# Kernel optimization log

Hardware: AMD Instinct MI355X
Metric: run time of the kernel (lower is better)

## Reference

```python
import jax, jax.numpy as jnp
import numpy as np

B, SQ, SK, H, A = 4, 512, 512, 256, 128

def setup_inputs() -> dict:
    key = jax.random.key(0)
    ks = jax.random.split(key, 8)
    s = 1.0 / np.sqrt(H)
    sa = 1.0 / np.sqrt(A)
    return {
        "Q": jax.random.normal(ks[0], (B, SQ, H), dtype=jnp.float32),
        "K": jax.random.normal(ks[1], (B, SK, H), dtype=jnp.float32),
        "V": jax.random.normal(ks[2], (B, SK, H), dtype=jnp.float32),
        "W_q": jax.random.uniform(ks[3], (H, A), jnp.float32, -s, s),
        "W_k": jax.random.uniform(ks[4], (H, A), jnp.float32, -s, s),
        "v": jax.random.uniform(ks[5], (A,), jnp.float32, -sa, sa),
        "W_o": jax.random.uniform(ks[6], (H, H), jnp.float32, -s, s),
        "b_o": jax.random.uniform(ks[7], (H,), jnp.float32, -s, s),
    }

def reference(Q, K, V, W_q, W_k, v, W_o, b_o):
    # Q: (B, Sq, H), K/V: (B, Sk, H)
    Qt = Q @ W_q                      # (B, Sq, A)
    Kt = K @ W_k                      # (B, Sk, A)
    additive = jnp.tanh(Qt[:, :, None, :] + Kt[:, None, :, :])  # (B, Sq, Sk, A)
    scores = jnp.einsum('bqka,a->bqk', additive, v)             # (B, Sq, Sk)
    weights = jax.nn.softmax(scores, axis=-1)                   # (B, Sq, Sk)
    out = jnp.einsum('bqk,bkh->bqh', weights, V)                 # (B, Sq, H)
    out = out @ W_o + b_o
    return (out, weights)
```

## Files before the change

kernel.cpp:

```cpp
#include <hip/hip_runtime.h>
#include <math.h>

#define BB 4
#define SQL 512
#define SKL 512
#define HH 256
#define AA 128

#define PRESCALE 2.8853900817779268f

__device__ inline void fma4(float4& a, float s, const float4& b) {
    a.x = fmaf(s, b.x, a.x); a.y = fmaf(s, b.y, a.y);
    a.z = fmaf(s, b.z, a.z); a.w = fmaf(s, b.w, a.w);
}

__global__ __launch_bounds__(256) void prep_kernel(
    const float* __restrict__ Q, const float* __restrict__ K,
    const float* __restrict__ V,
    const float* __restrict__ Wq, const float* __restrict__ Wk,
    const float* __restrict__ Wo,
    float* __restrict__ Qt, float* __restrict__ Kt, float* __restrict__ VW)
{
    __shared__ float rows[16 * HH];
    __shared__ float wl[64 * 128];
    int tid = threadIdx.x;
    int bid = blockIdx.x;

    const float* X; const float* W; float* Y;
    int ldW, ldY, col0, r0; float scale;
    if (bid < 128)      { X=Q; W=Wq; Y=Qt; ldW=AA; ldY=AA; col0=0; r0=bid*16;       scale=PRESCALE; }
    else if (bid < 256) { X=K; W=Wk; Y=Kt; ldW=AA; ldY=AA; col0=0; r0=(bid-128)*16; scale=PRESCALE; }
    else { int b2=bid-256; X=V; W=Wo; Y=VW; ldW=HH; ldY=HH; col0=(b2&1)*128; r0=(b2>>1)*16; scale=1.0f; }

    {
        const float4* Xv = (const float4*)(X + (size_t)r0 * HH);
        float4* rv = (float4*)rows;
        rv[tid]       = Xv[tid];
        rv[tid + 256] = Xv[tid + 256];
        rv[tid + 512] = Xv[tid + 512];
        rv[tid + 768] = Xv[tid + 768];
    }

    int r  = tid >> 5;
    int c4 = tid & 31;
    float4 accA = {0.f,0.f,0.f,0.f}, accB = {0.f,0.f,0.f,0.f};

    for (int ch = 0; ch < 4; ++ch) {
        __syncthreads();
        {
            const float* Wbase = W + (size_t)(ch * 64) * ldW + col0;
            float4* wv = (float4*)wl;
            #pragma unroll
            for (int it = 0; it < 8; ++it) {
                int l = tid + it * 256;
                wv[l] = *(const float4*)(Wbase + (size_t)(l >> 5) * ldW + ((l & 31) << 2));
            }
        }
        __syncthreads();
        const float* rrowA = rows + r * HH + ch * 64;
        const float* rrowB = rows + (r + 8) * HH + ch * 64;
        #pragma unroll 4
        for (int h4 = 0; h4 < 16; ++h4) {
            float4 ra = *(const float4*)(rrowA + h4 * 4);
            float4 rb = *(const float4*)(rrowB + h4 * 4);
            const float* wbase = wl + (h4 * 4) * 128 + (c4 << 2);
            float4 w0 = *(const float4*)(wbase);
            float4 w1 = *(const float4*)(wbase + 128);
            float4 w2 = *(const float4*)(wbase + 256);
            float4 w3 = *(const float4*)(wbase + 384);
            fma4(accA, ra.x, w0); fma4(accA, ra.y, w1);
            fma4(accA, ra.z, w2); fma4(accA, ra.w, w3);
            fma4(accB, rb.x, w0); fma4(accB, rb.y, w1);
            fma4(accB, rb.z, w2); fma4(accB, rb.w, w3);
        }
    }
    accA.x *= scale; accA.y *= scale; accA.z *= scale; accA.w *= scale;
    accB.x *= scale; accB.y *= scale; accB.z *= scale; accB.w *= scale;
    *(float4*)(Y + (size_t)(r0 + r)     * ldY + col0 + (c4 << 2)) = accA;
    *(float4*)(Y + (size_t)(r0 + r + 8) * ldY + col0 + (c4 << 2)) = accB;
}

__global__ __launch_bounds__(256) void score_kernel(
    const float* __restrict__ Qt, const float* __restrict__ Kt,
    const float* __restrict__ v,  const float* __restrict__ VW,
    const float* __restrict__ bo,
    float* __restrict__ weights,  float* __restrict__ out)
{
    __shared__ float score[2][SKL];
    __shared__ float pout[4][2][HH];

    int tid = threadIdx.x;
    int b  = blockIdx.x >> 8;
    int q0 = (blockIdx.x & 255) << 1;
    int ag = tid & 7;
    int kl = tid >> 3;

    float qreg0[16], qreg1[16], v2reg[16];
    {
        const float4* vp  = (const float4*)(v + ag * 16);
        const float4* qp0 = (const float4*)(Qt + (size_t)(b * SQL + q0)     * AA + ag * 16);
        const float4* qp1 = (const float4*)(Qt + (size_t)(b * SQL + q0 + 1) * AA + ag * 16);
        #pragma unroll
        for (int j4 = 0; j4 < 4; ++j4) {
            float4 vv4 = vp[j4];
            *(float4*)&qreg0[j4 * 4] = qp0[j4];
            *(float4*)&qreg1[j4 * 4] = qp1[j4];
            v2reg[j4 * 4 + 0] = 2.0f * vv4.x;
            v2reg[j4 * 4 + 1] = 2.0f * vv4.y;
            v2reg[j4 * 4 + 2] = 2.0f * vv4.z;
            v2reg[j4 * 4 + 3] = 2.0f * vv4.w;
        }
    }

    float S_all;
    {
        float ls = 0.f;
        #pragma unroll
        for (int j = 0; j < 16; ++j) ls += v2reg[j];
        ls += __shfl_xor(ls, 1);
        ls += __shfl_xor(ls, 2);
        ls += __shfl_xor(ls, 4);
        S_all = 0.5f * ls;
    }

    for (int c = 0; c < 16; ++c) {
        int k = c * 32 + kl;
        const float4* kt4 = (const float4*)(Kt + (size_t)(b * SKL + k) * AA + ag * 16);
        float kt[16];
        *(float4*)&kt[0]  = kt4[0];
        *(float4*)&kt[4]  = kt4[1];
        *(float4*)&kt[8]  = kt4[2];
        *(float4*)&kt[12] = kt4[3];

        float p0 = 0.f, p1 = 0.f;
        #pragma unroll
        for (int j = 0; j < 16; ++j) {
            float kv = kt[j];
            float x0 = qreg0[j] + kv;
            float x1 = qreg1[j] + kv;
            float e0 = __builtin_amdgcn_exp2f(x0);
            float e1 = __builtin_amdgcn_exp2f(x1);
            float r0 = __builtin_amdgcn_rcpf(e0 + 1.0f);
            float r1 = __builtin_amdgcn_rcpf(e1 + 1.0f);
            p0 = fmaf(v2reg[j], r0, p0);
            p1 = fmaf(v2reg[j], r1, p1);
        }
        p0 += __shfl_xor(p0, 1); p1 += __shfl_xor(p1, 1);
        p0 += __shfl_xor(p0, 2); p1 += __shfl_xor(p1, 2);
        p0 += __shfl_xor(p0, 4); p1 += __shfl_xor(p1, 4);
        if (ag == 0) {
            score[0][k] = S_all - p0;
            score[1][k] = S_all - p1;
        }
    }
    __syncthreads();

    int wave = tid >> 6, lane = tid & 63;
    if (wave < 2) {
        int qi = wave;
        float m = -1e30f;
        for (int k = lane; k < SKL; k += 64) m = fmaxf(m, score[qi][k]);
        #pragma unroll
        for (int off = 32; off; off >>= 1) m = fmaxf(m, __shfl_xor(m, off));
        float s = 0.f;
        for (int k = lane; k < SKL; k += 64) {
            float e = __builtin_amdgcn_exp2f((score[qi][k] - m) * 1.44269504f);
            score[qi][k] = e;
            s += e;
        }
        #pragma unroll
        for (int off = 32; off; off >>= 1) s += __shfl_xor(s, off);
        float rinv = 1.0f / s;
        size_t rowoff = (size_t)(b * SQL + q0 + qi) * SKL;
        for (int k = lane; k < SKL; k += 64) {
            float wv2 = score[qi][k] * rinv;
            score[qi][k] = wv2;
            weights[rowoff + k] = wv2;
        }
    }
    __syncthreads();

    {
        const float4* VWb = (const float4*)(VW + (size_t)b * SKL * HH);
        float4 a0 = {0,0,0,0}, a1 = {0,0,0,0};
        int kbase = wave * 128;
        #pragma unroll 4
        for (int k = 0; k < 128; ++k) {
            int kk = kbase + k;
            float4 vw4 = VWb[kk * (HH / 4) + lane];
            float w0 = score[0][kk];
            float w1 = score[1][kk];
            fma4(a0, w0, vw4);
            fma4(a1, w1, vw4);
        }
        *(float4*)&pout[wave][0][lane << 2] = a0;
        *(float4*)&pout[wave][1][lane << 2] = a1;
    }
    __syncthreads();
    {
        int h = tid;
        float bias = bo[h];
        #pragma unroll
        for (int qi = 0; qi < 2; ++qi) {
            float s = bias + pout[0][qi][h] + pout[1][qi][h]
                           + pout[2][qi][h] + pout[3][qi][h];
            out[(size_t)(b * SQL + q0 + qi) * HH + h] = s;
        }
    }
}

extern "C" void kernel_launch(void* const* d_in, const int* in_sizes, int n_in,
                              void* d_out, int out_size, void* d_ws, size_t ws_size,
                              hipStream_t stream)
{
    const float* Q  = (const float*)d_in[0];
    const float* K  = (const float*)d_in[1];
    const float* V  = (const float*)d_in[2];
    const float* Wq = (const float*)d_in[3];
    const float* Wk = (const float*)d_in[4];
    const float* v  = (const float*)d_in[5];
    const float* Wo = (const float*)d_in[6];
    const float* bo = (const float*)d_in[7];

    float* out     = (float*)d_out;
    float* weights = out + (size_t)BB * SQL * HH;

    float* Qt = (float*)d_ws;
    float* Kt = Qt + (size_t)BB * SQL * AA;
    float* VW = Kt + (size_t)BB * SKL * AA;

    prep_kernel <<<512, 256, 0, stream>>>(Q, K, V, Wq, Wk, Wo, Qt, Kt, VW);
    score_kernel<<<1024, 256, 0, stream>>>(Qt, Kt, v, VW, bo, weights, out);
}
```

Measured before the change: 129.8 us.

## Share exp across query pair, store VW in bf16, prefetch loads, parallelize softmax

In the score loop the second query's exp is computed as the first query's exp times a precomputed exp(q1-q0) factor, which removes one transcendental per element. Kt rows and W chunks are register-prefetched one iteration ahead to overlap loads with compute. The V@Wo intermediate is stored as bf16 to halve its memory traffic, at some cost in precision. Softmax now uses all four waves with float4 accesses and shared-memory partial reductions. The factored exp can overflow or lose accuracy when the two query rows differ a lot.

```diff
diff --git a/kernel.cpp b/kernel.cpp
--- a/kernel.cpp
+++ b/kernel.cpp
@@ -14,23 +14,37 @@
     a.z = fmaf(s, b.z, a.z); a.w = fmaf(s, b.w, a.w);
 }
 
+__device__ inline unsigned short f_to_bf16(float f) {
+    unsigned u = __float_as_uint(f);
+    return (unsigned short)((u + 0x7fffu + ((u >> 16) & 1u)) >> 16);
+}
+__device__ inline float4 bf16x4_to_f4(uint2 u) {
+    float4 r;
+    r.x = __uint_as_float(u.x << 16);
+    r.y = __uint_as_float(u.x & 0xffff0000u);
+    r.z = __uint_as_float(u.y << 16);
+    r.w = __uint_as_float(u.y & 0xffff0000u);
+    return r;
+}
+
 __global__ __launch_bounds__(256) void prep_kernel(
     const float* __restrict__ Q, const float* __restrict__ K,
     const float* __restrict__ V,
     const float* __restrict__ Wq, const float* __restrict__ Wk,
     const float* __restrict__ Wo,
-    float* __restrict__ Qt, float* __restrict__ Kt, float* __restrict__ VW)
+    float* __restrict__ Qt, float* __restrict__ Kt,
+    unsigned short* __restrict__ VW)
 {
     __shared__ float rows[16 * HH];
     __shared__ float wl[64 * 128];
     int tid = threadIdx.x;
     int bid = blockIdx.x;
 
-    const float* X; const float* W; float* Y;
-    int ldW, ldY, col0, r0; float scale;
-    if (bid < 128)      { X=Q; W=Wq; Y=Qt; ldW=AA; ldY=AA; col0=0; r0=bid*16;       scale=PRESCALE; }
-    else if (bid < 256) { X=K; W=Wk; Y=Kt; ldW=AA; ldY=AA; col0=0; r0=(bid-128)*16; scale=PRESCALE; }
-    else { int b2=bid-256; X=V; W=Wo; Y=VW; ldW=HH; ldY=HH; col0=(b2&1)*128; r0=(b2>>1)*16; scale=1.0f; }
+    const float* X; const float* W;
+    int ldW, col0, r0; float scale;
+    if (bid < 128)      { X=Q; W=Wq; ldW=AA; col0=0; r0=bid*16;       scale=PRESCALE; }
+    else if (bid < 256) { X=K; W=Wk; ldW=AA; col0=0; r0=(bid-128)*16; scale=PRESCALE; }
+    else { int b2=bid-256; X=V; W=Wo; ldW=HH; col0=(b2&1)*128; r0=(b2>>1)*16; scale=1.0f; }
 
     {
         const float4* Xv = (const float4*)(X + (size_t)r0 * HH);
@@ -41,6 +55,16 @@
         rv[tid + 768] = Xv[tid + 768];
     }
 
+    float4 wpf[8];
+    {
+        const float* Wb = W + col0;
+        #pragma unroll
+        for (int it = 0; it < 8; ++it) {
+            int l = tid + it * 256;
+            wpf[it] = *(const float4*)(Wb + (size_t)(l >> 5) * ldW + ((l & 31) << 2));
+        }
+    }
+
     int r  = tid >> 5;
     int c4 = tid & 31;
     float4 accA = {0.f,0.f,0.f,0.f}, accB = {0.f,0.f,0.f,0.f};
@@ -48,12 +72,16 @@
     for (int ch = 0; ch < 4; ++ch) {
         __syncthreads();
         {
-            const float* Wbase = W + (size_t)(ch * 64) * ldW + col0;
             float4* wv = (float4*)wl;
             #pragma unroll
-            for (int it = 0; it < 8; ++it) {
-                int l = tid + it * 256;
-                wv[l] = *(const float4*)(Wbase + (size_t)(l >> 5) * ldW + ((l & 31) << 2));
+            for (int it = 0; it < 8; ++it) wv[tid + it * 256] = wpf[it];
+            if (ch < 3) {
+                const float* Wb = W + (size_t)((ch + 1) * 64) * ldW + col0;
+                #pragma unroll
+                for (int it = 0; it < 8; ++it) {
+                    int l = tid + it * 256;
+                    wpf[it] = *(const float4*)(Wb + (size_t)(l >> 5) * ldW + ((l & 31) << 2));
+                }
             }
         }
         __syncthreads();
@@ -74,20 +102,32 @@
             fma4(accB, rb.z, w2); fma4(accB, rb.w, w3);
         }
     }
-    accA.x *= scale; accA.y *= scale; accA.z *= scale; accA.w *= scale;
-    accB.x *= scale; accB.y *= scale; accB.z *= scale; accB.w *= scale;
-    *(float4*)(Y + (size_t)(r0 + r)     * ldY + col0 + (c4 << 2)) = accA;
-    *(float4*)(Y + (size_t)(r0 + r + 8) * ldY + col0 + (c4 << 2)) = accB;
+
+    if (bid < 256) {
+        float* Y = (bid < 128) ? Qt : Kt;
+        accA.x *= scale; accA.y *= scale; accA.z *= scale; accA.w *= scale;
+        accB.x *= scale; accB.y *= scale; accB.z *= scale; accB.w *= scale;
+        *(float4*)(Y + (size_t)(r0 + r)     * AA + (c4 << 2)) = accA;
+        *(float4*)(Y + (size_t)(r0 + r + 8) * AA + (c4 << 2)) = accB;
+    } else {
+        ushort4 sa = { f_to_bf16(accA.x), f_to_bf16(accA.y),
+                       f_to_bf16(accA.z), f_to_bf16(accA.w) };
+        ushort4 sb = { f_to_bf16(accB.x), f_to_bf16(accB.y),
+                       f_to_bf16(accB.z), f_to_bf16(accB.w) };
+        *(ushort4*)(VW + (size_t)(r0 + r)     * HH + col0 + (c4 << 2)) = sa;
+        *(ushort4*)(VW + (size_t)(r0 + r + 8) * HH + col0 + (c4 << 2)) = sb;
+    }
 }
 
 __global__ __launch_bounds__(256) void score_kernel(
     const float* __restrict__ Qt, const float* __restrict__ Kt,
-    const float* __restrict__ v,  const float* __restrict__ VW,
+    const float* __restrict__ v,  const unsigned short* __restrict__ VW,
     const float* __restrict__ bo,
     float* __restrict__ weights,  float* __restrict__ out)
 {
     __shared__ float score[2][SKL];
     __shared__ float pout[4][2][HH];
+    __shared__ float pm[2][2], ps[2][2];
 
     int tid = threadIdx.x;
     int b  = blockIdx.x >> 8;
@@ -95,7 +135,7 @@
     int ag = tid & 7;
     int kl = tid >> 3;
 
-    float qreg0[16], qreg1[16], v2reg[16];
+    float qreg0[16], dreg[16], v2reg[16];
     {
         const float4* vp  = (const float4*)(v + ag * 16);
         const float4* qp0 = (const float4*)(Qt + (size_t)(b * SQL + q0)     * AA + ag * 16);
@@ -103,12 +143,17 @@
         #pragma unroll
         for (int j4 = 0; j4 < 4; ++j4) {
             float4 vv4 = vp[j4];
-            *(float4*)&qreg0[j4 * 4] = qp0[j4];
-            *(float4*)&qreg1[j4 * 4] = qp1[j4];
-            v2reg[j4 * 4 + 0] = 2.0f * vv4.x;
-            v2reg[j4 * 4 + 1] = 2.0f * vv4.y;
-            v2reg[j4 * 4 + 2] = 2.0f * vv4.z;
-            v2reg[j4 * 4 + 3] = 2.0f * vv4.w;
+            float4 a0  = qp0[j4];
+            float4 a1  = qp1[j4];
+            *(float4*)&qreg0[j4 * 4] = a0;
+            dreg[j4*4+0] = __builtin_amdgcn_exp2f(a1.x - a0.x);
+            dreg[j4*4+1] = __builtin_amdgcn_exp2f(a1.y - a0.y);
+            dreg[j4*4+2] = __builtin_amdgcn_exp2f(a1.z - a0.z);
+            dreg[j4*4+3] = __builtin_amdgcn_exp2f(a1.w - a0.w);
+            v2reg[j4*4+0] = 2.0f * vv4.x;
+            v2reg[j4*4+1] = 2.0f * vv4.y;
+            v2reg[j4*4+2] = 2.0f * vv4.z;
+            v2reg[j4*4+3] = 2.0f * vv4.w;
         }
     }
 
@@ -123,23 +168,25 @@
         S_all = 0.5f * ls;
     }
 
+    const float4* kp = (const float4*)(Kt + (size_t)(b * SKL + kl) * AA + ag * 16);
+    float4 n0 = kp[0], n1 = kp[1], n2 = kp[2], n3 = kp[3];
     for (int c = 0; c < 16; ++c) {
-        int k = c * 32 + kl;
-        const float4* kt4 = (const float4*)(Kt + (size_t)(b * SKL + k) * AA + ag * 16);
         float kt[16];
-        *(float4*)&kt[0]  = kt4[0];
-        *(float4*)&kt[4]  = kt4[1];
-        *(float4*)&kt[8]  = kt4[2];
-        *(float4*)&kt[12] = kt4[3];
+        *(float4*)&kt[0]  = n0;
+        *(float4*)&kt[4]  = n1;
+        *(float4*)&kt[8]  = n2;
+        *(float4*)&kt[12] = n3;
+        if (c < 15) {
+            const float4* np = kp + (size_t)(c + 1) * 32 * (AA / 4);
+            n0 = np[0]; n1 = np[1]; n2 = np[2]; n3 = np[3];
+        }
 
         float p0 = 0.f, p1 = 0.f;
         #pragma unroll
         for (int j = 0; j < 16; ++j) {
-            float kv = kt[j];
-            float x0 = qreg0[j] + kv;
-            float x1 = qreg1[j] + kv;
+            float x0 = qreg0[j] + kt[j];
             float e0 = __builtin_amdgcn_exp2f(x0);
-            float e1 = __builtin_amdgcn_exp2f(x1);
+            float e1 = e0 * dreg[j];
             float r0 = __builtin_amdgcn_rcpf(e0 + 1.0f);
             float r1 = __builtin_amdgcn_rcpf(e1 + 1.0f);
             p0 = fmaf(v2reg[j], r0, p0);
@@ -149,6 +196,7 @@
         p0 += __shfl_xor(p0, 2); p1 += __shfl_xor(p1, 2);
         p0 += __shfl_xor(p0, 4); p1 += __shfl_xor(p1, 4);
         if (ag == 0) {
+            int k = c * 32 + kl;
             score[0][k] = S_all - p0;
             score[1][k] = S_all - p1;
         }
@@ -156,38 +204,42 @@
     __syncthreads();
 
     int wave = tid >> 6, lane = tid & 63;
-    if (wave < 2) {
-        int qi = wave;
-        float m = -1e30f;
-        for (int k = lane; k < SKL; k += 64) m = fmaxf(m, score[qi][k]);
+    int qi = wave & 1, half = wave >> 1;
+    {
+        float4* srow = (float4*)&score[qi][half * 256];
+        float4 sv = srow[lane];
+        float m = fmaxf(fmaxf(sv.x, sv.y), fmaxf(sv.z, sv.w));
         #pragma unroll
         for (int off = 32; off; off >>= 1) m = fmaxf(m, __shfl_xor(m, off));
-        float s = 0.f;
-        for (int k = lane; k < SKL; k += 64) {
-            float e = __builtin_amdgcn_exp2f((score[qi][k] - m) * 1.44269504f);
-            score[qi][k] = e;
-            s += e;
-        }
+        if (lane == 0) pm[qi][half] = m;
+        __syncthreads();
+        float M = fmaxf(pm[qi][0], pm[qi][1]);
+        float4 e;
+        e.x = __builtin_amdgcn_exp2f((sv.x - M) * 1.44269504f);
+        e.y = __builtin_amdgcn_exp2f((sv.y - M) * 1.44269504f);
+        e.z = __builtin_amdgcn_exp2f((sv.z - M) * 1.44269504f);
+        e.w = __builtin_amdgcn_exp2f((sv.w - M) * 1.44269504f);
+        float s = (e.x + e.y) + (e.z + e.w);
         #pragma unroll
         for (int off = 32; off; off >>= 1) s += __shfl_xor(s, off);
-        float rinv = 1.0f / s;
-        size_t rowoff = (size_t)(b * SQL + q0 + qi) * SKL;
-        for (int k = lane; k < SKL; k += 64) {
-            float wv2 = score[qi][k] * rinv;
-            score[qi][k] = wv2;
-            weights[rowoff + k] = wv2;
-        }
+        if (lane == 0) ps[qi][half] = s;
+        __syncthreads();
+        float rinv = 1.0f / (ps[qi][0] + ps[qi][1]);
+        float4 w4 = { e.x * rinv, e.y * rinv, e.z * rinv, e.w * rinv };
+        srow[lane] = w4;
+        *(float4*)(weights + (size_t)(b * SQL + q0 + qi) * SKL + half * 256 + (lane << 2)) = w4;
     }
     __syncthreads();
 
     {
-        const float4* VWb = (const float4*)(VW + (size_t)b * SKL * HH);
+        const uint2* VWb = (const uint2*)(VW + (size_t)b * SKL * HH);
         float4 a0 = {0,0,0,0}, a1 = {0,0,0,0};
         int kbase = wave * 128;
         #pragma unroll 4
         for (int k = 0; k < 128; ++k) {
             int kk = kbase + k;
-            float4 vw4 = VWb[kk * (HH / 4) + lane];
+            uint2 u = VWb[(size_t)kk * (HH / 4) + lane];
+            float4 vw4 = bf16x4_to_f4(u);
             float w0 = score[0][kk];
             float w1 = score[1][kk];
             fma4(a0, w0, vw4);
@@ -201,10 +253,10 @@
         int h = tid;
         float bias = bo[h];
         #pragma unroll
-        for (int qi = 0; qi < 2; ++qi) {
-            float s = bias + pout[0][qi][h] + pout[1][qi][h]
-                           + pout[2][qi][h] + pout[3][qi][h];
-            out[(size_t)(b * SQL + q0 + qi) * HH + h] = s;
+        for (int qi2 = 0; qi2 < 2; ++qi2) {
+            float s = bias + pout[0][qi2][h] + pout[1][qi2][h]
+                           + pout[2][qi2][h] + pout[3][qi2][h];
+            out[(size_t)(b * SQL + q0 + qi2) * HH + h] = s;
         }
     }
 }
@@ -227,7 +279,7 @@
 
     float* Qt = (float*)d_ws;
     float* Kt = Qt + (size_t)BB * SQL * AA;
-    float* VW = Kt + (size_t)BB * SKL * AA;
+    unsigned short* VW = (unsigned short*)(Kt + (size_t)BB * SKL * AA);
 
     prep_kernel <<<512, 256, 0, stream>>>(Q, K, V, Wq, Wk, Wo, Qt, Kt, VW);
     score_kernel<<<1024, 256, 0, stream>>>(Qt, Kt, v, VW, bo, weights, out);
```

Result: slower. 138.9 us (+7.1%).
